# Kernel tuning notes

Hardware: AMD Instinct MI355X
Metric: run time of the kernel (lower is better)

## Reference

```python
import jax, jax.numpy as jnp
import numpy as np

E = 8          # num_experts
K = 2          # top-k
H = 768        # hidden_size
F = 4 * H      # FFN intermediate (expansion_factor=4)
B, S = 2, 2048


def setup_inputs() -> dict:
    key = jax.random.key(0)
    ks = jax.random.split(key, 5)
    scale = 0.02
    return {
        "x": jax.random.normal(ks[0], (B, S, H), dtype=jnp.float32),
        "router_w": jax.random.normal(ks[1], (H, E), dtype=jnp.float32) * scale,
        "router_b": jnp.zeros((E,), dtype=jnp.float32),
        "w1": jax.random.normal(ks[2], (E, H, F), dtype=jnp.float32) * scale,
        "b1": jnp.zeros((E, F), dtype=jnp.float32),
        "w2": jax.random.normal(ks[3], (E, F, H), dtype=jnp.float32) * scale,
        "b2": jnp.zeros((E, H), dtype=jnp.float32),
    }


def reference(x, router_w, router_b, w1, b1, w2, b2):
    b, s, h = x.shape
    # Router
    scores = jnp.einsum("bsh,he->bse", x, router_w) + router_b
    probs = jax.nn.softmax(scores, axis=-1)                      # [b,s,E]
    top_probs, expert_ids = jax.lax.top_k(probs, K)              # [b,s,K]

    # Load-balance auxiliary loss (Switch-style)
    avg_probs = probs.mean(axis=(0, 1))                          # [E]
    top1 = jnp.argmax(probs, axis=-1).reshape(-1)                # [b*s]
    counts = jnp.zeros((E,), dtype=probs.dtype).at[top1].add(1.0)
    expert_freqs = counts / (b * s)
    bal_loss = 0.001 * jnp.dot(expert_freqs, avg_probs)

    # Normalize top-k gate weights
    norm_probs = top_probs / (top_probs.sum(axis=-1, keepdims=True) + 1e-9)  # [b,s,K]

    # Expert FFNs with ReLU^2 activation, computed per-expert (dense, then masked)
    h1 = jnp.einsum("bsh,ehf->ebsf", x, w1) + b1[:, None, None, :]
    h1 = jnp.square(jax.nn.relu(h1))
    h2 = jnp.einsum("ebsf,efh->ebsh", h1, w2) + b2[:, None, None, :]  # [E,b,s,H]

    # Combine: weight for expert e at token (b,s) = sum_k norm_probs * 1[ids_k == e]
    onehot = jax.nn.one_hot(expert_ids, E, dtype=x.dtype)        # [b,s,K,E]
    gate = jnp.einsum("bsk,bske->ebs", norm_probs, onehot)       # [E,b,s]
    out = jnp.einsum("ebs,ebsh->bsh", gate, h2)                  # [b,s,H]
    return out, bal_loss
```

## Files before the change

### kernel.cpp

```cpp
#include <hip/hip_runtime.h>
#include <hip/hip_bf16.h>
#include <stdint.h>

#define E_EXP 8
#define TOK   4096
#define HD    768
#define FD    3072
#define BK    64
#define CAP   8320

typedef __attribute__((ext_vector_type(8))) short bf16x8;
typedef __attribute__((ext_vector_type(4))) float f32x4;

__device__ __forceinline__ unsigned short f2bf(float f) {
  union { float f; unsigned u; } v; v.f = f;
  unsigned r = v.u + 0x7fffu + ((v.u >> 16) & 1u);
  return (unsigned short)(r >> 16);
}
__device__ __forceinline__ float bf2f(unsigned short u) {
  union { unsigned u; float f; } v; v.u = ((unsigned)u) << 16;
  return v.f;
}

__device__ __forceinline__ void gload_lds16(const void* g, void* l) {
  __builtin_amdgcn_global_load_lds(
      (const __attribute__((address_space(1))) unsigned int*)g,
      (__attribute__((address_space(3))) unsigned int*)l, 16, 0, 0);
}

__device__ __forceinline__ int xcd_swizzle(int orig, int nwg) {
  int xcd = orig & 7, base = orig >> 3;
  int q = nwg >> 3, r = nwg & 7;
  return (xcd < r ? xcd * (q + 1) : r * (q + 1) + (xcd - r) * q) + base;
}

__global__ __launch_bounds__(256) void router_kernel(
    const float* __restrict__ x, const float* __restrict__ rw,
    const float* __restrict__ rb, unsigned short* __restrict__ xb,
    float* __restrict__ probs, int* __restrict__ ids,
    float* __restrict__ gates)
{
  __shared__ float lrw[E_EXP * HD];
  for (int i = threadIdx.x; i < E_EXP * HD; i += 256) {
    int h = i >> 3, e = i & 7;
    lrw[e * HD + h] = rw[i];
  }
  __syncthreads();
  const int wave = threadIdx.x >> 6, lane = threadIdx.x & 63;
  const int t = blockIdx.x * 4 + wave;
  const float* xrow = x + (size_t)t * HD;
  float acc[8] = {0, 0, 0, 0, 0, 0, 0, 0};
#pragma unroll
  for (int i = 0; i < HD / 64; ++i) {
    int h = i * 64 + lane;
    float xv = xrow[h];
    xb[(size_t)t * HD + h] = f2bf(xv);
#pragma unroll
    for (int e = 0; e < 8; ++e) acc[e] += xv * lrw[e * HD + h];
  }
#pragma unroll
  for (int d = 1; d < 64; d <<= 1) {
#pragma unroll
    for (int e = 0; e < 8; ++e) acc[e] += __shfl_xor(acc[e], d);
  }
  if (lane == 0) {
    float p[8]; float m = -1e30f, sum = 0.f;
#pragma unroll
    for (int e = 0; e < 8; ++e) { p[e] = acc[e] + rb[e]; m = fmaxf(m, p[e]); }
#pragma unroll
    for (int e = 0; e < 8; ++e) { p[e] = __expf(p[e] - m); sum += p[e]; }
    float inv = 1.f / sum;
#pragma unroll
    for (int e = 0; e < 8; ++e) p[e] *= inv;
    int i1 = 0;
#pragma unroll
    for (int e = 1; e < 8; ++e) if (p[e] > p[i1]) i1 = e;
    int i2 = (i1 == 0) ? 1 : 0;
#pragma unroll
    for (int e = 0; e < 8; ++e) if (e != i1 && p[e] > p[i2]) i2 = e;
    ids[t * 2] = i1; ids[t * 2 + 1] = i2;
    float den = 1.f / (p[i1] + p[i2] + 1e-9f);
    gates[t * 2] = p[i1] * den; gates[t * 2 + 1] = p[i2] * den;
#pragma unroll
    for (int e = 0; e < 8; ++e) probs[t * 8 + e] = p[e];
  }
}

__global__ __launch_bounds__(256) void transpose_kernel(
    const float* __restrict__ W, unsigned short* __restrict__ Wt,
    int Kd, int Nd)
{
  __shared__ float tile[32][33];
  const int e = blockIdx.z;
  const int n0 = blockIdx.x * 32, k0 = blockIdx.y * 32;
  const int ci = threadIdx.x & 31, ri = threadIdx.x >> 5;
  const float* src = W + ((size_t)e * Kd + k0) * Nd + n0;
#pragma unroll
  for (int i = 0; i < 32; i += 8)
    tile[ri + i][ci] = src[(size_t)(ri + i) * Nd + ci];
  __syncthreads();
  unsigned short* dst = Wt + ((size_t)e * Nd + n0) * Kd + k0;
  const int co = (threadIdx.x & 15) * 2, ro = threadIdx.x >> 4;
#pragma unroll
  for (int i = 0; i < 32; i += 16) {
    int r = ro + i;
    unsigned v = (unsigned)f2bf(tile[co][r]) | ((unsigned)f2bf(tile[co + 1][r]) << 16);
    *(unsigned*)&dst[(size_t)r * Kd + co] = v;
  }
}

__global__ __launch_bounds__(256) void stats_kernel(
    const int* __restrict__ ids, const float* __restrict__ probs,
    int* __restrict__ meta, float* __restrict__ loss_out)
{
  __shared__ int cnt[8], top1c[8];
  __shared__ float wsum[4][8];
  if (threadIdx.x < 8) { cnt[threadIdx.x] = 0; top1c[threadIdx.x] = 0; }
  __syncthreads();
  float local[8] = {0, 0, 0, 0, 0, 0, 0, 0};
  for (int t = threadIdx.x; t < TOK; t += 256) {
    int e0 = ids[2 * t], e1 = ids[2 * t + 1];
    atomicAdd(&cnt[e0], 1); atomicAdd(&cnt[e1], 1); atomicAdd(&top1c[e0], 1);
    const float4* pr = (const float4*)&probs[(size_t)t * 8];
    float4 a = pr[0], b = pr[1];
    local[0] += a.x; local[1] += a.y; local[2] += a.z; local[3] += a.w;
    local[4] += b.x; local[5] += b.y; local[6] += b.z; local[7] += b.w;
  }
#pragma unroll
  for (int d = 1; d < 64; d <<= 1) {
#pragma unroll
    for (int e = 0; e < 8; ++e) local[e] += __shfl_xor(local[e], d);
  }
  const int wave = threadIdx.x >> 6, lane = threadIdx.x & 63;
  if (lane == 0) {
#pragma unroll
    for (int e = 0; e < 8; ++e) wsum[wave][e] = local[e];
  }
  __syncthreads();
  if (threadIdx.x == 0) {
    int total = 0, nt1 = 0, nt2 = 0;
    for (int e = 0; e < 8; ++e) {
      int c = cnt[e];
      meta[e] = c;
      meta[16 + e] = total;
      int t1 = (c + 127) >> 7;
      for (int i = 0; i < t1; ++i) { meta[64 + nt1 * 2] = e; meta[64 + nt1 * 2 + 1] = total + i * 128; ++nt1; }
      int t2 = (c + 63) >> 6;
      for (int i = 0; i < t2; ++i) { meta[256 + nt2 * 2] = e; meta[256 + nt2 * 2 + 1] = total + i * 64; ++nt2; }
      total += c;
    }
    meta[32] = nt1; meta[33] = nt2;
    float loss = 0.f;
    for (int e = 0; e < 8; ++e) {
      float psum = wsum[0][e] + wsum[1][e] + wsum[2][e] + wsum[3][e];
      loss += ((float)top1c[e] / 4096.f) * (psum / 4096.f);
    }
    loss_out[0] = 0.001f * loss;
  }
}

__global__ __launch_bounds__(256) void scatter_kernel(
    const int* __restrict__ ids, int* __restrict__ meta,
    int* __restrict__ token_list, int* __restrict__ pos_list)
{
  __shared__ int lcnt[8];
  __shared__ int lbase[8];
  if (threadIdx.x < 8) lcnt[threadIdx.x] = 0;
  __syncthreads();
  const int t = blockIdx.x * 256 + threadIdx.x;
  const int e0 = ids[t * 2], e1 = ids[t * 2 + 1];
  const int s0 = atomicAdd(&lcnt[e0], 1);
  const int s1 = atomicAdd(&lcnt[e1], 1);
  __syncthreads();
  if (threadIdx.x < 8)
    lbase[threadIdx.x] = atomicAdd(&meta[24 + threadIdx.x], lcnt[threadIdx.x]);
  __syncthreads();
  int p0 = meta[16 + e0] + lbase[e0] + s0;
  int p1 = meta[16 + e1] + lbase[e1] + s1;
  token_list[p0] = t; pos_list[t * 2] = p0;
  token_list[p1] = t; pos_list[t * 2 + 1] = p1;
}

template<int BM, int BN, int MODE, int NW>
__global__ __launch_bounds__(NW * 64, 4) void moe_gemm(
    const unsigned short* __restrict__ A,
    const unsigned short* __restrict__ Bw,
    const float* __restrict__ bias,
    const int* __restrict__ token_list,
    const int* __restrict__ meta,
    unsigned short* __restrict__ Cout,
    const int Kdim, const int NN)
{
  const int NY = NN / BN;
  const int wgid = xcd_swizzle(blockIdx.x, gridDim.x);
  const int mt = wgid / NY;
  const int ny = wgid - mt * NY;
  const int nt_total = meta[32 + MODE];
  if (mt >= nt_total) return;
  const int* tmap = meta + (MODE == 0 ? 64 : 256);
  const int e = tmap[mt * 2], arow0 = tmap[mt * 2 + 1];
  const int ne_end = meta[16 + e] + meta[e];
  const int n0 = ny * BN;

  __shared__ unsigned short lA[BM * BK];
  __shared__ unsigned short lB[BN * BK];

  const int tid = threadIdx.x;
  const int wave = tid >> 6, lane = tid & 63;
  constexpr int WC_N = NW / 2;
  const int wr = wave / WC_N, wc = wave % WC_N;
  constexpr int WROWS = BM / 2;
  constexpr int WCOLS = BN / WC_N;
  constexpr int FM = WROWS / 16, FN = WCOLS / 16;
  constexpr int NCA = (BM / 8) / NW;
  constexpr int NCB = (BN / 8) / NW;

  const int kswz = ((lane & 7) ^ ((lane >> 3) & 7)) * 8;

  size_t aSrc[NCA];
#pragma unroll
  for (int i = 0; i < NCA; ++i) {
    int c = wave + i * NW;
    int r = c * 8 + (lane >> 3);
    int grow = (MODE == 0) ? token_list[arow0 + r] : (arow0 + r);
    aSrc[i] = (size_t)grow * Kdim + kswz;
  }
  size_t bSrc[NCB];
#pragma unroll
  for (int i = 0; i < NCB; ++i) {
    int c = wave + i * NW;
    int n = n0 + c * 8 + (lane >> 3);
    bSrc[i] = ((size_t)e * NN + n) * Kdim + kswz;
  }

  f32x4 acc[FM][FN] = {};

  for (int k0 = 0; k0 < Kdim; k0 += BK) {
#pragma unroll
    for (int i = 0; i < NCA; ++i)
      gload_lds16(A + aSrc[i] + k0, &lA[(wave + i * NW) * 512]);
#pragma unroll
    for (int i = 0; i < NCB; ++i)
      gload_lds16(Bw + bSrc[i] + k0, &lB[(wave + i * NW) * 512]);
    __syncthreads();
#pragma unroll
    for (int kk = 0; kk < BK; kk += 32) {
      bf16x8 af[FM], bfr[FN];
      const int lc = (kk >> 3) + (lane >> 4);
#pragma unroll
      for (int m2 = 0; m2 < FM; ++m2) {
        int row = wr * WROWS + m2 * 16 + (lane & 15);
        af[m2] = *(const bf16x8*)&lA[row * BK + ((lc ^ (row & 7)) << 3)];
      }
#pragma unroll
      for (int n2 = 0; n2 < FN; ++n2) {
        int row = wc * WCOLS + n2 * 16 + (lane & 15);
        bfr[n2] = *(const bf16x8*)&lB[row * BK + ((lc ^ (row & 7)) << 3)];
      }
#pragma unroll
      for (int m2 = 0; m2 < FM; ++m2)
#pragma unroll
        for (int n2 = 0; n2 < FN; ++n2)
          acc[m2][n2] = __builtin_amdgcn_mfma_f32_16x16x32_bf16(
              af[m2], bfr[n2], acc[m2][n2], 0, 0, 0);
    }
    __syncthreads();
  }

  const float* be = bias + (size_t)e * NN;
#pragma unroll
  for (int m2 = 0; m2 < FM; ++m2) {
    const int lr = wr * WROWS + m2 * 16 + (lane >> 4) * 4;
#pragma unroll
    for (int n2 = 0; n2 < FN; ++n2) {
      const int col = n0 + wc * WCOLS + n2 * 16 + (lane & 15);
      const float bv = be[col];
#pragma unroll
      for (int j = 0; j < 4; ++j) {
        const int arow = arow0 + lr + j;
        if (arow < ne_end) {
          float v = acc[m2][n2][j] + bv;
          if (MODE == 0) { v = fmaxf(v, 0.f); v = v * v; }
          Cout[(size_t)arow * NN + col] = f2bf(v);
        }
      }
    }
  }
}

__global__ __launch_bounds__(256) void combine_kernel(
    const unsigned short* __restrict__ h2, const int* __restrict__ pos_list,
    const float* __restrict__ gates, float* __restrict__ out)
{
  const int wave = threadIdx.x >> 6, lane = threadIdx.x & 63;
  const int t = blockIdx.x * 4 + wave;
  const int p0 = pos_list[2 * t], p1 = pos_list[2 * t + 1];
  const float g0 = gates[2 * t], g1 = gates[2 * t + 1];
  const unsigned short* r0 = h2 + (size_t)p0 * HD;
  const unsigned short* r1 = h2 + (size_t)p1 * HD;
  float* o = out + (size_t)t * HD;
#pragma unroll
  for (int i = 0; i < 3; ++i) {
    int h = i * 256 + lane * 4;
    ushort4 a = *(const ushort4*)&r0[h];
    ushort4 b = *(const ushort4*)&r1[h];
    float4 o4;
    o4.x = g0 * bf2f(a.x) + g1 * bf2f(b.x);
    o4.y = g0 * bf2f(a.y) + g1 * bf2f(b.y);
    o4.z = g0 * bf2f(a.z) + g1 * bf2f(b.z);
    o4.w = g0 * bf2f(a.w) + g1 * bf2f(b.w);
    *(float4*)&o[h] = o4;
  }
}

extern "C" void kernel_launch(void* const* d_in, const int* in_sizes, int n_in,
                              void* d_out, int out_size, void* d_ws, size_t ws_size,
                              hipStream_t stream)
{
  (void)in_sizes; (void)n_in; (void)ws_size; (void)out_size;
  const float* x  = (const float*)d_in[0];
  const float* rw = (const float*)d_in[1];
  const float* rb = (const float*)d_in[2];
  const float* w1 = (const float*)d_in[3];
  const float* b1 = (const float*)d_in[4];
  const float* w2 = (const float*)d_in[5];
  const float* b2 = (const float*)d_in[6];
  float* out = (float*)d_out;

  char* ws = (char*)d_ws;
  size_t off = 0;
  auto alloc = [&](size_t bytes) {
    off = (off + 255) & ~(size_t)255;
    void* p = ws + off;
    off += bytes;
    return p;
  };
  unsigned short* xb  = (unsigned short*)alloc((size_t)TOK * HD * 2);
  unsigned short* w1t = (unsigned short*)alloc((size_t)E_EXP * FD * HD * 2);
  unsigned short* w2t = (unsigned short*)alloc((size_t)E_EXP * HD * FD * 2);
  unsigned short* h1  = (unsigned short*)alloc((size_t)CAP * FD * 2);
  unsigned short* h2  = (unsigned short*)alloc((size_t)CAP * HD * 2);
  int*   token_list = (int*)alloc(CAP * 4);
  int*   pos_list   = (int*)alloc((size_t)TOK * 2 * 4);
  int*   ids        = (int*)alloc((size_t)TOK * 2 * 4);
  float* gates      = (float*)alloc((size_t)TOK * 2 * 4);
  float* probs      = (float*)alloc((size_t)TOK * 8 * 4);
  int*   meta       = (int*)alloc(1024 * 4);
  char*  ctrl       = (char*)token_list;
  size_t ctrl_bytes = (ws + off) - ctrl;

  hipMemsetAsync(ctrl, 0, ctrl_bytes, stream);

  router_kernel<<<TOK / 4, 256, 0, stream>>>(x, rw, rb, xb, probs, ids, gates);
  transpose_kernel<<<dim3(FD / 32, HD / 32, E_EXP), 256, 0, stream>>>(w1, w1t, HD, FD);
  transpose_kernel<<<dim3(HD / 32, FD / 32, E_EXP), 256, 0, stream>>>(w2, w2t, FD, HD);
  stats_kernel<<<1, 256, 0, stream>>>(ids, probs, meta, out + (size_t)TOK * HD);
  scatter_kernel<<<TOK / 256, 256, 0, stream>>>(ids, meta, token_list, pos_list);
  moe_gemm<128, 128, 0, 4><<<71 * (FD / 128), 256, 0, stream>>>(
      xb, w1t, b1, token_list, meta, h1, HD, FD);
  moe_gemm<64, 128, 1, 4><<<135 * (HD / 128), 256, 0, stream>>>(
      h1, w2t, b2, token_list, meta, h2, FD, HD);
  combine_kernel<<<TOK / 4, 256, 0, stream>>>(h2, pos_list, gates, out);
}
```

Measured before the change: 210.2 us.

## Split-K the second expert GEMM with 128-row tiles and merge weight transposes

The second MoE GEMM now uses 128x128 tiles, the same tile map as the first GEMM, and splits its K dimension (3072) into two halves. Each half writes a bf16 partial result to its own h2 buffer, and the combine kernel sums the two partials before applying the gate weights. The two weight-transpose launches are merged into one kernel with a flat grid. The aim is to keep the CU count busy with larger tiles and fewer launches, at the cost of doubled h2 traffic and an extra bf16 rounding of the partial sums.

```diff
diff --git a/kernel.cpp b/kernel.cpp
--- a/kernel.cpp
+++ b/kernel.cpp
@@ -86,13 +86,25 @@
   }
 }
 
+#define W1_TILES (E_EXP * (FD / 32) * (HD / 32))
+#define W2_TILES (E_EXP * (HD / 32) * (FD / 32))
 __global__ __launch_bounds__(256) void transpose_kernel(
-    const float* __restrict__ W, unsigned short* __restrict__ Wt,
-    int Kd, int Nd)
+    const float* __restrict__ w1, unsigned short* __restrict__ w1t,
+    const float* __restrict__ w2, unsigned short* __restrict__ w2t)
 {
   __shared__ float tile[32][33];
-  const int e = blockIdx.z;
-  const int n0 = blockIdx.x * 32, k0 = blockIdx.y * 32;
+  int id = blockIdx.x;
+  const float* W; unsigned short* Wt; int Kd, Nd;
+  if (id < W1_TILES) {
+    W = w1; Wt = w1t; Kd = HD; Nd = FD;
+  } else {
+    id -= W1_TILES; W = w2; Wt = w2t; Kd = FD; Nd = HD;
+  }
+  const int nx = Nd / 32;
+  const int e = id / (nx * (Kd / 32));
+  const int rem = id % (nx * (Kd / 32));
+  const int n0 = (rem % nx) * 32, k0 = (rem / nx) * 32;
+
   const int ci = threadIdx.x & 31, ri = threadIdx.x >> 5;
   const float* src = W + ((size_t)e * Kd + k0) * Nd + n0;
 #pragma unroll
@@ -138,18 +150,16 @@
   }
   __syncthreads();
   if (threadIdx.x == 0) {
-    int total = 0, nt1 = 0, nt2 = 0;
+    int total = 0, nt1 = 0;
     for (int e = 0; e < 8; ++e) {
       int c = cnt[e];
       meta[e] = c;
       meta[16 + e] = total;
       int t1 = (c + 127) >> 7;
       for (int i = 0; i < t1; ++i) { meta[64 + nt1 * 2] = e; meta[64 + nt1 * 2 + 1] = total + i * 128; ++nt1; }
-      int t2 = (c + 63) >> 6;
-      for (int i = 0; i < t2; ++i) { meta[256 + nt2 * 2] = e; meta[256 + nt2 * 2 + 1] = total + i * 64; ++nt2; }
       total += c;
     }
-    meta[32] = nt1; meta[33] = nt2;
+    meta[32] = nt1;
     float loss = 0.f;
     for (int e = 0; e < 8; ++e) {
       float psum = wsum[0][e] + wsum[1][e] + wsum[2][e] + wsum[3][e];
@@ -181,7 +191,7 @@
   token_list[p1] = t; pos_list[t * 2 + 1] = p1;
 }
 
-template<int BM, int BN, int MODE, int NW>
+template<int BM, int BN, int MODE, int NW, int NKP>
 __global__ __launch_bounds__(NW * 64, 4) void moe_gemm(
     const unsigned short* __restrict__ A,
     const unsigned short* __restrict__ Bw,
@@ -193,14 +203,19 @@
 {
   const int NY = NN / BN;
   const int wgid = xcd_swizzle(blockIdx.x, gridDim.x);
-  const int mt = wgid / NY;
-  const int ny = wgid - mt * NY;
-  const int nt_total = meta[32 + MODE];
+  const int mt = wgid / (NY * NKP);
+  const int slot = wgid - mt * (NY * NKP);
+  const int ny = slot % NY;
+  const int kp = slot / NY;
+  const int nt_total = meta[32];
   if (mt >= nt_total) return;
-  const int* tmap = meta + (MODE == 0 ? 64 : 256);
+  const int* tmap = meta + 64;
   const int e = tmap[mt * 2], arow0 = tmap[mt * 2 + 1];
   const int ne_end = meta[16 + e] + meta[e];
   const int n0 = ny * BN;
+  const int KLEN = Kdim / NKP;
+  const int kbeg = kp * KLEN;
+  unsigned short* Cp = Cout + (size_t)kp * CAP * NN;
 
   __shared__ unsigned short lA[BM * BK];
   __shared__ unsigned short lB[BN * BK];
@@ -223,19 +238,19 @@
     int c = wave + i * NW;
     int r = c * 8 + (lane >> 3);
     int grow = (MODE == 0) ? token_list[arow0 + r] : (arow0 + r);
-    aSrc[i] = (size_t)grow * Kdim + kswz;
+    aSrc[i] = (size_t)grow * Kdim + kbeg + kswz;
   }
   size_t bSrc[NCB];
 #pragma unroll
   for (int i = 0; i < NCB; ++i) {
     int c = wave + i * NW;
     int n = n0 + c * 8 + (lane >> 3);
-    bSrc[i] = ((size_t)e * NN + n) * Kdim + kswz;
+    bSrc[i] = ((size_t)e * NN + n) * Kdim + kbeg + kswz;
   }
 
   f32x4 acc[FM][FN] = {};
 
-  for (int k0 = 0; k0 < Kdim; k0 += BK) {
+  for (int k0 = 0; k0 < KLEN; k0 += BK) {
 #pragma unroll
     for (int i = 0; i < NCA; ++i)
       gload_lds16(A + aSrc[i] + k0, &lA[(wave + i * NW) * 512]);
@@ -274,14 +289,14 @@
 #pragma unroll
     for (int n2 = 0; n2 < FN; ++n2) {
       const int col = n0 + wc * WCOLS + n2 * 16 + (lane & 15);
-      const float bv = be[col];
+      const float bv = (kp == 0) ? be[col] : 0.f;
 #pragma unroll
       for (int j = 0; j < 4; ++j) {
         const int arow = arow0 + lr + j;
         if (arow < ne_end) {
           float v = acc[m2][n2][j] + bv;
           if (MODE == 0) { v = fmaxf(v, 0.f); v = v * v; }
-          Cout[(size_t)arow * NN + col] = f2bf(v);
+          Cp[(size_t)arow * NN + col] = f2bf(v);
         }
       }
     }
@@ -292,23 +307,28 @@
     const unsigned short* __restrict__ h2, const int* __restrict__ pos_list,
     const float* __restrict__ gates, float* __restrict__ out)
 {
+  const unsigned short* h2b = h2 + (size_t)CAP * HD;
   const int wave = threadIdx.x >> 6, lane = threadIdx.x & 63;
   const int t = blockIdx.x * 4 + wave;
   const int p0 = pos_list[2 * t], p1 = pos_list[2 * t + 1];
   const float g0 = gates[2 * t], g1 = gates[2 * t + 1];
-  const unsigned short* r0 = h2 + (size_t)p0 * HD;
-  const unsigned short* r1 = h2 + (size_t)p1 * HD;
+  const unsigned short* r0a = h2  + (size_t)p0 * HD;
+  const unsigned short* r0b = h2b + (size_t)p0 * HD;
+  const unsigned short* r1a = h2  + (size_t)p1 * HD;
+  const unsigned short* r1b = h2b + (size_t)p1 * HD;
   float* o = out + (size_t)t * HD;
 #pragma unroll
   for (int i = 0; i < 3; ++i) {
     int h = i * 256 + lane * 4;
-    ushort4 a = *(const ushort4*)&r0[h];
-    ushort4 b = *(const ushort4*)&r1[h];
+    ushort4 a0 = *(const ushort4*)&r0a[h];
+    ushort4 b0 = *(const ushort4*)&r0b[h];
+    ushort4 a1 = *(const ushort4*)&r1a[h];
+    ushort4 b1 = *(const ushort4*)&r1b[h];
     float4 o4;
-    o4.x = g0 * bf2f(a.x) + g1 * bf2f(b.x);
-    o4.y = g0 * bf2f(a.y) + g1 * bf2f(b.y);
-    o4.z = g0 * bf2f(a.z) + g1 * bf2f(b.z);
-    o4.w = g0 * bf2f(a.w) + g1 * bf2f(b.w);
+    o4.x = g0 * (bf2f(a0.x) + bf2f(b0.x)) + g1 * (bf2f(a1.x) + bf2f(b1.x));
+    o4.y = g0 * (bf2f(a0.y) + bf2f(b0.y)) + g1 * (bf2f(a1.y) + bf2f(b1.y));
+    o4.z = g0 * (bf2f(a0.z) + bf2f(b0.z)) + g1 * (bf2f(a1.z) + bf2f(b1.z));
+    o4.w = g0 * (bf2f(a0.w) + bf2f(b0.w)) + g1 * (bf2f(a1.w) + bf2f(b1.w));
     *(float4*)&o[h] = o4;
   }
 }
@@ -339,7 +359,7 @@
   unsigned short* w1t = (unsigned short*)alloc((size_t)E_EXP * FD * HD * 2);
   unsigned short* w2t = (unsigned short*)alloc((size_t)E_EXP * HD * FD * 2);
   unsigned short* h1  = (unsigned short*)alloc((size_t)CAP * FD * 2);
-  unsigned short* h2  = (unsigned short*)alloc((size_t)CAP * HD * 2);
+  unsigned short* h2  = (unsigned short*)alloc((size_t)2 * CAP * HD * 2);
   int*   token_list = (int*)alloc(CAP * 4);
   int*   pos_list   = (int*)alloc((size_t)TOK * 2 * 4);
   int*   ids        = (int*)alloc((size_t)TOK * 2 * 4);
@@ -352,13 +372,12 @@
   hipMemsetAsync(ctrl, 0, ctrl_bytes, stream);
 
   router_kernel<<<TOK / 4, 256, 0, stream>>>(x, rw, rb, xb, probs, ids, gates);
-  transpose_kernel<<<dim3(FD / 32, HD / 32, E_EXP), 256, 0, stream>>>(w1, w1t, HD, FD);
-  transpose_kernel<<<dim3(HD / 32, FD / 32, E_EXP), 256, 0, stream>>>(w2, w2t, FD, HD);
+  transpose_kernel<<<W1_TILES + W2_TILES, 256, 0, stream>>>(w1, w1t, w2, w2t);
   stats_kernel<<<1, 256, 0, stream>>>(ids, probs, meta, out + (size_t)TOK * HD);
   scatter_kernel<<<TOK / 256, 256, 0, stream>>>(ids, meta, token_list, pos_list);
-  moe_gemm<128, 128, 0, 4><<<71 * (FD / 128), 256, 0, stream>>>(
+  moe_gemm<128, 128, 0, 4, 1><<<71 * (FD / 128), 256, 0, stream>>>(
       xb, w1t, b1, token_list, meta, h1, HD, FD);
-  moe_gemm<64, 128, 1, 4><<<135 * (HD / 128), 256, 0, stream>>>(
+  moe_gemm<128, 128, 1, 4, 2><<<71 * (HD / 128) * 2, 256, 0, stream>>>(
       h1, w2t, b2, token_list, meta, h2, FD, HD);
   combine_kernel<<<TOK / 4, 256, 0, stream>>>(h2, pos_list, gates, out);
 }
```

Result: faster. 201.8 us (-4.0%).
